# Performance work log

Measured on AMD Instinct MI355X. Metric: run time of the kernel, lower is better.

The kernel has to match this reference:

```python
import jax, jax.numpy as jnp
import numpy as np


def setup_inputs() -> dict:
    key = jax.random.key(0)
    ks = jax.random.split(key, 12)
    N, D, E = 50000, 64, 320000
    H0, H1, H2, OUT = 4 * D, 128, 128, 1  # edgemlp_size=[256,128,128], out_features=1
    h1 = jax.random.normal(ks[0], (N, D), dtype=jnp.float32)
    h2 = jax.random.normal(ks[1], (N, D), dtype=jnp.float32)
    src = jax.random.randint(ks[2], (E,), 0, N, dtype=jnp.int64)
    dst = jax.random.randint(ks[3], (E,), 0, N, dtype=jnp.int64)
    def lin_init(kw, kb, fan_in, fan_out):
        bound = 1.0 / np.sqrt(fan_in)
        W = jax.random.uniform(kw, (fan_out, fan_in), minval=-bound, maxval=bound, dtype=jnp.float32)
        b = jax.random.uniform(kb, (fan_out,), minval=-bound, maxval=bound, dtype=jnp.float32)
        return W, b
    W1, b1 = lin_init(ks[4], ks[5], H0, H1)
    W2, b2 = lin_init(ks[6], ks[7], H1, H2)
    W3, b3 = lin_init(ks[8], ks[9], H2, OUT)
    return {"h1": h1, "h2": h2, "src": src, "dst": dst,
            "W1": W1, "b1": b1, "W2": W2, "b2": b2, "W3": W3, "b3": b3}


def reference(h1, h2, src, dst, W1, b1, W2, b2, W3, b3):
    # Gather per-edge node features. NOTE: original code uses edges.src['h2']
    # for BOTH h2_u and h2_v (faithful to source), so h2 is gathered by src twice.
    h1_u = h1[src]            # [E, D]
    h1_v = h1[dst]            # [E, D]
    h2_u = h2[src]            # [E, D]
    h2_v = h2[src]            # [E, D]  (src, per original)
    h = jnp.concatenate([h1_u, h1_v, h2_u, h2_v], axis=1)  # [E, 4D]
    h = jax.nn.sigmoid(h @ W1.T + b1)
    h = jax.nn.sigmoid(h @ W2.T + b2)
    score = h @ W3.T + b3     # [E, out_features]
    return score
```

## Files before the change

kernel.cpp:

```cpp
#include <hip/hip_runtime.h>
#include <hip/hip_bf16.h>
#include <cstdint>


typedef __attribute__((ext_vector_type(8))) short bf16x8;
typedef __attribute__((ext_vector_type(4))) float f32x4;

__device__ __forceinline__ float sigmoid_fast(float x) {
    float e = __expf(-x);
    return __builtin_amdgcn_rcpf(1.0f + e);
}
__device__ __forceinline__ ushort f2bf_rne(float f) {
    uint32_t u = __float_as_uint(f);
    return (ushort)((u + 0x7fffu + ((u >> 16) & 1u)) >> 16);
}
__device__ __forceinline__ float bf2f_lo(uint32_t d) { return __uint_as_float(d << 16); }
__device__ __forceinline__ float bf2f_hi(uint32_t d) { return __uint_as_float(d & 0xffff0000u); }
__device__ __forceinline__ uint32_t packbf_rhu(float x, float y) {
    return ((__float_as_uint(x) + 0x8000u) >> 16) |
           ((__float_as_uint(y) + 0x8000u) & 0xffff0000u);
}

__global__ void prep_kernel(const float* __restrict__ W1, const float* __restrict__ W2,
                            ushort* __restrict__ WCF, ushort* __restrict__ WBF,
                            ushort* __restrict__ W2F) {
    int i = blockIdx.x * blockDim.x + threadIdx.x;
    if (i >= 16384) return;
    int j = i & 7, lf = (i >> 3) & 63, nt = (i >> 9) & 7, kk = i >> 12;
    int n = nt * 16 + (lf & 15);
    int kpos = kk * 32 + ((lf >> 4) << 3) + j;
    int ktrue = (kpos & ~31) | ((kpos >> 1) & 15) | ((kpos & 1) << 4);
    W2F[i] = f2bf_rne(W2[n * 128 + ktrue]);
    float v = (kpos < 64) ? W1[n * 256 + kpos]
                          : W1[n * 256 + 128 + (kpos - 64)] + W1[n * 256 + 192 + (kpos - 64)];
    WCF[i] = f2bf_rne(v);
    if (kk < 2) WBF[i] = f2bf_rne(W1[n * 256 + 64 + kpos]);
}

__global__ __launch_bounds__(256, 4) void node_kernel(
    const float* __restrict__ h1, const float* __restrict__ h2,
    const ushort* __restrict__ WCF, const ushort* __restrict__ WBF,
    const float* __restrict__ b1,
    uint32_t* __restrict__ Aout, uint32_t* __restrict__ Bout, int N)
{
    __shared__ __align__(16) ushort xt[64 * 136];
    const int tid = threadIdx.x, g = tid >> 6, ln = tid & 63;
    const int nl = ln & 15, q = ln >> 4;
    const int n0 = blockIdx.x * 64;
    const bool full = (n0 + 64 <= N);

    bf16x8 fa[4][2], fb[2][2];
    #pragma unroll
    for (int kk = 0; kk < 4; ++kk)
        #pragma unroll
        for (int nt = 0; nt < 2; ++nt)
            fa[kk][nt] = *(const bf16x8*)(WCF + (((kk * 8 + g * 2 + nt) * 64 + ln) << 3));
    #pragma unroll
    for (int kk = 0; kk < 2; ++kk)
        #pragma unroll
        for (int nt = 0; nt < 2; ++nt)
            fb[kk][nt] = *(const bf16x8*)(WBF + (((kk * 8 + g * 2 + nt) * 64 + ln) << 3));
    const float b1c0 = b1[g * 32 + nl], b1c1 = b1[g * 32 + 16 + nl];

    #pragma unroll
    for (int i = 0; i < 8; ++i) {
        int local = i * 256 + tid;
        int node = local >> 5;
        int kq = (local & 31) * 4;
        float4 x = make_float4(0.f, 0.f, 0.f, 0.f);
        if (full || n0 + node < N)
            x = (kq < 64) ? *(const float4*)(h1 + (size_t)(n0 + node) * 64 + kq)
                          : *(const float4*)(h2 + (size_t)(n0 + node) * 64 + (kq - 64));
        uint32_t d0 = packbf_rhu(x.x, x.y), d1 = packbf_rhu(x.z, x.w);
        *(uint2*)&xt[node * 136 + kq] = make_uint2(d0, d1);
    }
    __syncthreads();

    #pragma unroll
    for (int m = 0; m < 4; ++m) {
        f32x4 accA[2], accB[2];
        #pragma unroll
        for (int r = 0; r < 4; ++r) { accA[0][r] = accA[1][r] = accB[0][r] = accB[1][r] = 0.f; }
        const ushort* arow = &xt[(m * 16 + nl) * 136 + (q << 3)];
        #pragma unroll
        for (int kk = 0; kk < 4; ++kk) {
            bf16x8 a = *(const bf16x8*)(arow + kk * 32);
            accA[0] = __builtin_amdgcn_mfma_f32_16x16x32_bf16(a, fa[kk][0], accA[0], 0, 0, 0);
            accA[1] = __builtin_amdgcn_mfma_f32_16x16x32_bf16(a, fa[kk][1], accA[1], 0, 0, 0);
            if (kk < 2) {
                accB[0] = __builtin_amdgcn_mfma_f32_16x16x32_bf16(a, fb[kk][0], accB[0], 0, 0, 0);
                accB[1] = __builtin_amdgcn_mfma_f32_16x16x32_bf16(a, fb[kk][1], accB[1], 0, 0, 0);
            }
        }
        #pragma unroll
        for (int r = 0; r < 4; ++r) {
            int node = n0 + m * 16 + q * 4 + r;
            if (full || node < N) {
                Aout[(size_t)node * 64 + g * 16 + nl] = packbf_rhu(accA[0][r] + b1c0, accA[1][r] + b1c1);
                Bout[(size_t)node * 64 + g * 16 + nl] = packbf_rhu(accB[0][r], accB[1][r]);
            }
        }
    }
}

__global__ __launch_bounds__(256, 4) void edge_kernel(
    const uint32_t* __restrict__ Am, const uint32_t* __restrict__ Bm,
    const int* __restrict__ src, const int* __restrict__ dst,
    const ushort* __restrict__ W2F, const float* __restrict__ b2,
    const float* __restrict__ W3, const float* __restrict__ b3,
    float* __restrict__ out, int E, int ntiles)
{
    __shared__ __align__(16) ushort hlds[2][64 * 136];
    __shared__ float part[2][256];
    const int tid = threadIdx.x, g = tid >> 6, ln = tid & 63;
    const int nl = ln & 15, q = ln >> 4;
    const int el = g * 16 + (ln >> 2);
    const int p  = ln & 3;

    bf16x8 bfrag[8];
    #pragma unroll
    for (int kk = 0; kk < 4; ++kk)
        #pragma unroll
        for (int nt = 0; nt < 2; ++nt)
            bfrag[kk * 2 + nt] =
                *(const bf16x8*)(W2F + (((kk * 8 + g * 2 + nt) * 64 + ln) << 3));
    float b2c[2], w3c[2];
    #pragma unroll
    for (int nt = 0; nt < 2; ++nt) {
        int n = g * 32 + nt * 16 + nl;
        b2c[nt] = b2[n]; w3c[nt] = W3[n];
    }
    const float b3c = b3[0];

    uint4 ga[4], gb[4];
    int t = blockIdx.x;
    if (t < ntiles) {
        int eb = t * 64 + g * 16, us = 0, vs = 0;
        if (ln < 16 && eb + ln < E) { us = src[eb + ln]; vs = dst[eb + ln]; }
        int uu = __shfl(us, ln >> 2), vv = __shfl(vs, ln >> 2);
        const uint32_t* ap = Am + (size_t)uu * 64 + p * 4;
        const uint32_t* bp = Bm + (size_t)vv * 64 + p * 4;
        #pragma unroll
        for (int r = 0; r < 4; ++r) {
            ga[r] = *(const uint4*)(ap + r * 16);
            gb[r] = *(const uint4*)(bp + r * 16);
        }
    }
    int buf = 0, prev = -1;
    for (; t < ntiles; t += gridDim.x) {
        #pragma unroll
        for (int r = 0; r < 4; ++r) {
            uint32_t sa[4] = {ga[r].x, ga[r].y, ga[r].z, ga[r].w};
            uint32_t sb[4] = {gb[r].x, gb[r].y, gb[r].z, gb[r].w};
            uint32_t da[4];
            #pragma unroll
            for (int d = 0; d < 4; ++d) {
                float zl = bf2f_lo(sa[d]) + bf2f_lo(sb[d]);
                float zh = bf2f_hi(sa[d]) + bf2f_hi(sb[d]);
                da[d] = packbf_rhu(sigmoid_fast(zl), sigmoid_fast(zh));
            }
            *(uint4*)&hlds[buf][el * 136 + r * 32 + p * 8] =
                make_uint4(da[0], da[1], da[2], da[3]);
        }
        int tn = t + gridDim.x;
        if (tn < ntiles) {
            int eb = tn * 64 + g * 16, us = 0, vs = 0;
            if (ln < 16 && eb + ln < E) { us = src[eb + ln]; vs = dst[eb + ln]; }
            int uu = __shfl(us, ln >> 2), vv = __shfl(vs, ln >> 2);
            const uint32_t* ap = Am + (size_t)uu * 64 + p * 4;
            const uint32_t* bp = Bm + (size_t)vv * 64 + p * 4;
            #pragma unroll
            for (int r = 0; r < 4; ++r) {
                ga[r] = *(const uint4*)(ap + r * 16);
                gb[r] = *(const uint4*)(bp + r * 16);
            }
        }
        __syncthreads();

        if (prev >= 0 && tid < 64) {
            int e = prev * 64 + tid;
            if (e < E)
                out[e] = (part[buf ^ 1][tid] + part[buf ^ 1][64 + tid])
                       + (part[buf ^ 1][128 + tid] + part[buf ^ 1][192 + tid]) + b3c;
        }

        #pragma unroll
        for (int m = 0; m < 4; ++m) {
            f32x4 acc[2];
            #pragma unroll
            for (int r = 0; r < 4; ++r) { acc[0][r] = 0.f; acc[1][r] = 0.f; }
            const ushort* arow = &hlds[buf][(m * 16 + nl) * 136 + (q << 3)];
            #pragma unroll
            for (int kk = 0; kk < 4; ++kk) {
                bf16x8 a = *(const bf16x8*)(arow + kk * 32);
                acc[0] = __builtin_amdgcn_mfma_f32_16x16x32_bf16(a, bfrag[kk * 2],     acc[0], 0, 0, 0);
                acc[1] = __builtin_amdgcn_mfma_f32_16x16x32_bf16(a, bfrag[kk * 2 + 1], acc[1], 0, 0, 0);
            }
            float pr[4] = {0.f, 0.f, 0.f, 0.f};
            #pragma unroll
            for (int nt = 0; nt < 2; ++nt)
                #pragma unroll
                for (int r = 0; r < 4; ++r)
                    pr[r] = fmaf(w3c[nt], sigmoid_fast(acc[nt][r] + b2c[nt]), pr[r]);
            #pragma unroll
            for (int r = 0; r < 4; ++r) {
                pr[r] += __shfl_xor(pr[r], 1, 16);
                pr[r] += __shfl_xor(pr[r], 2, 16);
                pr[r] += __shfl_xor(pr[r], 4, 16);
                pr[r] += __shfl_xor(pr[r], 8, 16);
            }
            if (nl == 0) {
                #pragma unroll
                for (int r = 0; r < 4; ++r)
                    part[buf][g * 64 + m * 16 + q * 4 + r] = pr[r];
            }
        }
        prev = t; buf ^= 1;
    }
    __syncthreads();
    if (prev >= 0 && tid < 64) {
        int e = prev * 64 + tid;
        if (e < E)
            out[e] = (part[buf ^ 1][tid] + part[buf ^ 1][64 + tid])
                   + (part[buf ^ 1][128 + tid] + part[buf ^ 1][192 + tid]) + b3c;
    }
}

__global__ void naive_kernel(
    const float* __restrict__ h1, const float* __restrict__ h2,
    const int* __restrict__ src, const int* __restrict__ dst,
    const float* __restrict__ W1, const float* __restrict__ b1,
    const float* __restrict__ W2, const float* __restrict__ b2,
    const float* __restrict__ W3, const float* __restrict__ b3,
    float* __restrict__ out, int E, int N)
{
    int e = blockIdx.x * blockDim.x + threadIdx.x;
    if (e >= E) return;
    int u = src[e], v = dst[e];
    float h[128];
    for (int j = 0; j < 128; ++j) {
        float z = b1[j];
        const float* wj = W1 + j * 256;
        for (int k = 0; k < 64; ++k) {
            z += wj[k] * h1[(size_t)u * 64 + k]
               + wj[64 + k] * h1[(size_t)v * 64 + k]
               + (wj[128 + k] + wj[192 + k]) * h2[(size_t)u * 64 + k];
        }
        h[j] = 1.0f / (1.0f + __expf(-z));
    }
    float gg[128];
    for (int j = 0; j < 128; ++j) {
        float z = b2[j];
        for (int k = 0; k < 128; ++k) z = fmaf(W2[j * 128 + k], h[k], z);
        gg[j] = 1.0f / (1.0f + __expf(-z));
    }
    float s = b3[0];
    for (int j = 0; j < 128; ++j) s = fmaf(W3[j], gg[j], s);
    out[e] = s;
}

extern "C" void kernel_launch(void* const* d_in, const int* in_sizes, int n_in,
                              void* d_out, int out_size, void* d_ws, size_t ws_size,
                              hipStream_t stream) {
    const float* h1 = (const float*)d_in[0];
    const float* h2 = (const float*)d_in[1];
    const int*  src = (const int*)d_in[2];
    const int*  dst = (const int*)d_in[3];
    const float* W1 = (const float*)d_in[4];
    const float* b1 = (const float*)d_in[5];
    const float* W2 = (const float*)d_in[6];
    const float* b2 = (const float*)d_in[7];
    const float* W3 = (const float*)d_in[8];
    const float* b3 = (const float*)d_in[9];
    float* out = (float*)d_out;

    const int N = in_sizes[0] / 64;
    const int E = in_sizes[2];

    size_t offA   = 0;
    size_t offB   = offA + (size_t)N * 64;
    size_t offWCF = offB + (size_t)N * 64;
    size_t offWBF = offWCF + 8192;
    size_t offW2F = offWBF + 4096;
    size_t totalF = offW2F + 8192;

    if (ws_size < totalF * sizeof(float)) {
        naive_kernel<<<(E + 255) / 256, 256, 0, stream>>>(
            h1, h2, src, dst, W1, b1, W2, b2, W3, b3, out, E, N);
        return;
    }

    float* ws = (float*)d_ws;
    ushort* WCF = (ushort*)(ws + offWCF);
    ushort* WBF = (ushort*)(ws + offWBF);
    ushort* W2F = (ushort*)(ws + offW2F);

    prep_kernel<<<64, 256, 0, stream>>>(W1, W2, WCF, WBF, W2F);
    node_kernel<<<(N + 63) / 64, 256, 0, stream>>>(
        h1, h2, WCF, WBF, b1, (uint32_t*)(ws + offA), (uint32_t*)(ws + offB), N);
    const int ntiles = (E + 63) / 64;
    edge_kernel<<<2500, 256, 0, stream>>>(
        (const uint32_t*)(ws + offA), (const uint32_t*)(ws + offB), src, dst,
        W2F, b2, W3, b3, out, E, ntiles);
}
```

Baseline: 130.8 us.

## Restructure edge kernel so each single-wave block computes all outputs for 16 edges

The edge kernel changes from 256-thread blocks, where four waves each cover a quarter of the hidden units, to 64-thread blocks where one wave holds all of W2 in registers and computes every output for 16 edges. This removes the block barrier, the double-buffered LDS partial-sum exchange, and the cross-wave reduction. Each wave now writes its outputs directly as a float4, and the src/dst index loads for the next group are issued earlier in the loop. In exchange, register use per wave rises sharply (32 bf16x8 fragments), and the grid of 2000 single-wave blocks means fewer waves in flight to hide gather latency.

```diff
diff --git a/kernel.cpp b/kernel.cpp
--- a/kernel.cpp
+++ b/kernel.cpp
@@ -103,41 +103,39 @@
     }
 }
 
-__global__ __launch_bounds__(256, 4) void edge_kernel(
+__global__ __launch_bounds__(64, 2) void edge_kernel(
     const uint32_t* __restrict__ Am, const uint32_t* __restrict__ Bm,
     const int* __restrict__ src, const int* __restrict__ dst,
     const ushort* __restrict__ W2F, const float* __restrict__ b2,
     const float* __restrict__ W3, const float* __restrict__ b3,
-    float* __restrict__ out, int E, int ntiles)
+    float* __restrict__ out, int E, int ngroups)
 {
-    __shared__ __align__(16) ushort hlds[2][64 * 136];
-    __shared__ float part[2][256];
-    const int tid = threadIdx.x, g = tid >> 6, ln = tid & 63;
+    __shared__ __align__(16) ushort hlds[16 * 136];
+    const int ln = threadIdx.x;
     const int nl = ln & 15, q = ln >> 4;
-    const int el = g * 16 + (ln >> 2);
-    const int p  = ln & 3;
-
-    bf16x8 bfrag[8];
+    const int el = ln >> 2, p = ln & 3;
+
+    bf16x8 bfrag[32];
     #pragma unroll
     for (int kk = 0; kk < 4; ++kk)
         #pragma unroll
-        for (int nt = 0; nt < 2; ++nt)
-            bfrag[kk * 2 + nt] =
-                *(const bf16x8*)(W2F + (((kk * 8 + g * 2 + nt) * 64 + ln) << 3));
-    float b2c[2], w3c[2];
-    #pragma unroll
-    for (int nt = 0; nt < 2; ++nt) {
-        int n = g * 32 + nt * 16 + nl;
-        b2c[nt] = b2[n]; w3c[nt] = W3[n];
+        for (int nt = 0; nt < 8; ++nt)
+            bfrag[kk * 8 + nt] =
+                *(const bf16x8*)(W2F + (((kk * 8 + nt) * 64 + ln) << 3));
+    float b2c[8], w3c[8];
+    #pragma unroll
+    for (int nt = 0; nt < 8; ++nt) {
+        b2c[nt] = b2[nt * 16 + nl];
+        w3c[nt] = W3[nt * 16 + nl];
     }
     const float b3c = b3[0];
 
     uint4 ga[4], gb[4];
-    int t = blockIdx.x;
-    if (t < ntiles) {
-        int eb = t * 64 + g * 16, us = 0, vs = 0;
+    int grp = blockIdx.x;
+    if (grp < ngroups) {
+        int eb = grp * 16, us = 0, vs = 0;
         if (ln < 16 && eb + ln < E) { us = src[eb + ln]; vs = dst[eb + ln]; }
-        int uu = __shfl(us, ln >> 2), vv = __shfl(vs, ln >> 2);
+        int uu = __shfl(us, el), vv = __shfl(vs, el);
         const uint32_t* ap = Am + (size_t)uu * 64 + p * 4;
         const uint32_t* bp = Bm + (size_t)vv * 64 + p * 4;
         #pragma unroll
@@ -146,8 +144,14 @@
             gb[r] = *(const uint4*)(bp + r * 16);
         }
     }
-    int buf = 0, prev = -1;
-    for (; t < ntiles; t += gridDim.x) {
+    for (; grp < ngroups; grp += gridDim.x) {
+        const int tn = grp + (int)gridDim.x;
+        int us = 0, vs = 0;
+        if (tn < ngroups) {
+            int eb2 = tn * 16;
+            if (ln < 16 && eb2 + ln < E) { us = src[eb2 + ln]; vs = dst[eb2 + ln]; }
+        }
+
         #pragma unroll
         for (int r = 0; r < 4; ++r) {
             uint32_t sa[4] = {ga[r].x, ga[r].y, ga[r].z, ga[r].w};
@@ -159,14 +163,11 @@
                 float zh = bf2f_hi(sa[d]) + bf2f_hi(sb[d]);
                 da[d] = packbf_rhu(sigmoid_fast(zl), sigmoid_fast(zh));
             }
-            *(uint4*)&hlds[buf][el * 136 + r * 32 + p * 8] =
+            *(uint4*)&hlds[el * 136 + r * 32 + p * 8] =
                 make_uint4(da[0], da[1], da[2], da[3]);
         }
-        int tn = t + gridDim.x;
-        if (tn < ntiles) {
-            int eb = tn * 64 + g * 16, us = 0, vs = 0;
-            if (ln < 16 && eb + ln < E) { us = src[eb + ln]; vs = dst[eb + ln]; }
-            int uu = __shfl(us, ln >> 2), vv = __shfl(vs, ln >> 2);
+        if (tn < ngroups) {
+            int uu = __shfl(us, el), vv = __shfl(vs, el);
             const uint32_t* ap = Am + (size_t)uu * 64 + p * 4;
             const uint32_t* bp = Bm + (size_t)vv * 64 + p * 4;
             #pragma unroll
@@ -175,54 +176,50 @@
                 gb[r] = *(const uint4*)(bp + r * 16);
             }
         }
-        __syncthreads();
-
-        if (prev >= 0 && tid < 64) {
-            int e = prev * 64 + tid;
-            if (e < E)
-                out[e] = (part[buf ^ 1][tid] + part[buf ^ 1][64 + tid])
-                       + (part[buf ^ 1][128 + tid] + part[buf ^ 1][192 + tid]) + b3c;
-        }
-
-        #pragma unroll
-        for (int m = 0; m < 4; ++m) {
-            f32x4 acc[2];
+
+        const ushort* arow = &hlds[nl * 136 + (q << 3)];
+        bf16x8 a0 = *(const bf16x8*)(arow);
+        bf16x8 a1 = *(const bf16x8*)(arow + 32);
+        bf16x8 a2 = *(const bf16x8*)(arow + 64);
+        bf16x8 a3 = *(const bf16x8*)(arow + 96);
+
+        float pr[4] = {0.f, 0.f, 0.f, 0.f};
+        #pragma unroll
+        for (int np = 0; np < 4; ++np) {
+            const int n0t = 2 * np, n1t = 2 * np + 1;
+            f32x4 acc0 = {0.f, 0.f, 0.f, 0.f}, acc1 = {0.f, 0.f, 0.f, 0.f};
+            acc0 = __builtin_amdgcn_mfma_f32_16x16x32_bf16(a0, bfrag[n0t],      acc0, 0, 0, 0);
+            acc1 = __builtin_amdgcn_mfma_f32_16x16x32_bf16(a0, bfrag[n1t],      acc1, 0, 0, 0);
+            acc0 = __builtin_amdgcn_mfma_f32_16x16x32_bf16(a1, bfrag[8 + n0t],  acc0, 0, 0, 0);
+            acc1 = __builtin_amdgcn_mfma_f32_16x16x32_bf16(a1, bfrag[8 + n1t],  acc1, 0, 0, 0);
+            acc0 = __builtin_amdgcn_mfma_f32_16x16x32_bf16(a2, bfrag[16 + n0t], acc0, 0, 0, 0);
+            acc1 = __builtin_amdgcn_mfma_f32_16x16x32_bf16(a2, bfrag[16 + n1t], acc1, 0, 0, 0);
+            acc0 = __builtin_amdgcn_mfma_f32_16x16x32_bf16(a3, bfrag[24 + n0t], acc0, 0, 0, 0);
+            acc1 = __builtin_amdgcn_mfma_f32_16x16x32_bf16(a3, bfrag[24 + n1t], acc1, 0, 0, 0);
             #pragma unroll
-            for (int r = 0; r < 4; ++r) { acc[0][r] = 0.f; acc[1][r] = 0.f; }
-            const ushort* arow = &hlds[buf][(m * 16 + nl) * 136 + (q << 3)];
-            #pragma unroll
-            for (int kk = 0; kk < 4; ++kk) {
-                bf16x8 a = *(const bf16x8*)(arow + kk * 32);
-                acc[0] = __builtin_amdgcn_mfma_f32_16x16x32_bf16(a, bfrag[kk * 2],     acc[0], 0, 0, 0);
-                acc[1] = __builtin_amdgcn_mfma_f32_16x16x32_bf16(a, bfrag[kk * 2 + 1], acc[1], 0, 0, 0);
-            }
-            float pr[4] = {0.f, 0.f, 0.f, 0.f};
-            #pragma unroll
-            for (int nt = 0; nt < 2; ++nt)
+            for (int r = 0; r < 4; ++r) {
+                pr[r] = fmaf(w3c[n0t], sigmoid_fast(acc0[r] + b2c[n0t]), pr[r]);
+                pr[r] = fmaf(w3c[n1t], sigmoid_fast(acc1[r] + b2c[n1t]), pr[r]);
+            }
+        }
+        #pragma unroll
+        for (int r = 0; r < 4; ++r) {
+            pr[r] += __shfl_xor(pr[r], 1, 16);
+            pr[r] += __shfl_xor(pr[r], 2, 16);
+            pr[r] += __shfl_xor(pr[r], 4, 16);
+            pr[r] += __shfl_xor(pr[r], 8, 16);
+        }
+        if (nl == 0) {
+            int eo = grp * 16 + q * 4;
+            if (eo + 4 <= E) {
+                *(float4*)(out + eo) = make_float4(pr[0] + b3c, pr[1] + b3c,
+                                                   pr[2] + b3c, pr[3] + b3c);
+            } else {
                 #pragma unroll
                 for (int r = 0; r < 4; ++r)
-                    pr[r] = fmaf(w3c[nt], sigmoid_fast(acc[nt][r] + b2c[nt]), pr[r]);
-            #pragma unroll
-            for (int r = 0; r < 4; ++r) {
-                pr[r] += __shfl_xor(pr[r], 1, 16);
-                pr[r] += __shfl_xor(pr[r], 2, 16);
-                pr[r] += __shfl_xor(pr[r], 4, 16);
-                pr[r] += __shfl_xor(pr[r], 8, 16);
-            }
-            if (nl == 0) {
-                #pragma unroll
-                for (int r = 0; r < 4; ++r)
-                    part[buf][g * 64 + m * 16 + q * 4 + r] = pr[r];
-            }
-        }
-        prev = t; buf ^= 1;
-    }
-    __syncthreads();
-    if (prev >= 0 && tid < 64) {
-        int e = prev * 64 + tid;
-        if (e < E)
-            out[e] = (part[buf ^ 1][tid] + part[buf ^ 1][64 + tid])
-                   + (part[buf ^ 1][128 + tid] + part[buf ^ 1][192 + tid]) + b3c;
+                    if (eo + r < E) out[eo + r] = pr[r] + b3c;
+            }
+        }
     }
 }
 
@@ -298,8 +295,8 @@
     prep_kernel<<<64, 256, 0, stream>>>(W1, W2, WCF, WBF, W2F);
     node_kernel<<<(N + 63) / 64, 256, 0, stream>>>(
         h1, h2, WCF, WBF, b1, (uint32_t*)(ws + offA), (uint32_t*)(ws + offB), N);
-    const int ntiles = (E + 63) / 64;
-    edge_kernel<<<2500, 256, 0, stream>>>(
+    const int ngroups = (E + 15) / 16;
+    edge_kernel<<<2000, 64, 0, stream>>>(
         (const uint32_t*)(ws + offA), (const uint32_t*)(ws + offB), src, dst,
-        W2F, b2, W3, b3, out, E, ntiles);
-}
+        W2F, b2, W3, b3, out, E, ngroups);
+}
```

Result: no change. 132.2 us (+1.1%).
